# Optimization experiments

Measured on AMD Instinct MI355X. Metric: run time of the kernel, lower is better.

The kernel has to match this reference:

```python
import jax, jax.numpy as jnp
import numpy as np

D_MODEL, N_HEADS, KV_LAT, VOCAB = 2048, 16, 512, 32000
DH = D_MODEL // N_HEADS
ROPE_BASE = 20000.0
LN_EPS = 1e-5


def _layernorm(x, g, b):
    mu = jnp.mean(x, axis=-1, keepdims=True)
    var = jnp.var(x, axis=-1, keepdims=True)
    return (x - mu) * jax.lax.rsqrt(var + LN_EPS) * g + b


def _rope(x):
    # standard half-split rotary embedding over the last dim (d_model), base=20000
    B, S, D = x.shape
    half = D // 2
    inv_freq = 1.0 / (ROPE_BASE ** (jnp.arange(half, dtype=jnp.float32) / half))
    ang = jnp.arange(S, dtype=jnp.float32)[:, None] * inv_freq[None, :]  # [S, half]
    cos, sin = jnp.cos(ang), jnp.sin(ang)
    x1, x2 = x[..., :half], x[..., half:]
    return jnp.concatenate([x1 * cos - x2 * sin, x1 * sin + x2 * cos], axis=-1)


def setup_inputs() -> dict:
    key = jax.random.key(0)
    ks = jax.random.split(key, 10)
    s = 0.02
    return {
        "x": jax.random.normal(ks[0], (1, 2048, D_MODEL), dtype=jnp.float32),
        # Linear weights stored as [in, out] so y = x @ W
        "W_dq": jax.random.normal(ks[1], (D_MODEL, KV_LAT), dtype=jnp.float32) * s,
        "W_dkv": jax.random.normal(ks[2], (D_MODEL, KV_LAT), dtype=jnp.float32) * s,
        "W_uk": jax.random.normal(ks[3], (KV_LAT, D_MODEL), dtype=jnp.float32) * s,
        "W_uv": jax.random.normal(ks[4], (KV_LAT, D_MODEL), dtype=jnp.float32) * s,
        "W_uq": jax.random.normal(ks[5], (KV_LAT, D_MODEL), dtype=jnp.float32) * s,
        "W_qr": jax.random.normal(ks[6], (KV_LAT, D_MODEL), dtype=jnp.float32) * s,
        "W_kr": jax.random.normal(ks[7], (D_MODEL, DH), dtype=jnp.float32) * s,
        "W_o": jax.random.normal(ks[8], (D_MODEL, VOCAB), dtype=jnp.float32) * s,
        "g_kv": jnp.ones((KV_LAT,), dtype=jnp.float32),
        "b_kv": jnp.zeros((KV_LAT,), dtype=jnp.float32),
        "g_kr": jnp.ones((DH,), dtype=jnp.float32),
        "b_kr": jnp.zeros((DH,), dtype=jnp.float32),
    }


def reference(x, W_dq, W_dkv, W_uk, W_uv, W_uq, W_qr, W_kr, W_o,
              g_kv, b_kv, g_kr, b_kr):
    B, S, D = x.shape
    # query latent and up-projection
    c_q = _layernorm(x @ W_dq, g_kv, b_kv)                      # [B,S,kv]
    q_c = (c_q @ W_uq).reshape(B, S, N_HEADS, DH)               # [B,S,H,dh]
    # kv latent cache (no past cache -> just this chunk)
    c_kv = _layernorm(x @ W_dkv, g_kv, b_kv)                    # [B,S,kv]
    k_c = (c_kv @ W_uk).reshape(B, S, N_HEADS, DH)
    v_c = (c_kv @ W_uv).reshape(B, S, N_HEADS, DH)
    # decoupled RoPE paths (RoPE applied only to q, as in source)
    q_r = _rope(c_q @ W_qr).reshape(B, S, N_HEADS, DH)
    k_r = _layernorm(x @ W_kr, g_kr, b_kr)                      # [B,S,dh]
    k_r_h = jnp.broadcast_to(k_r[:, :, None, :], (B, S, N_HEADS, DH))
    q = jnp.concatenate([q_c, q_r], axis=3)                     # [B,S,H,2dh]
    k = jnp.concatenate([k_c, k_r_h], axis=3)                   # [B,S,H,2dh]
    scores = jnp.einsum("bqhd,bkhd->bhqk", q, k) / np.sqrt(2.0 * DH)
    causal = jnp.tril(jnp.ones((S, S), dtype=bool))             # past_length=0
    scores = jnp.where(causal[None, None], scores, -jnp.inf)
    attn = jax.nn.softmax(scores, axis=-1)
    out_heads = jnp.einsum("bhqk,bkhd->bqhd", attn, v_c).reshape(B, S, D)
    out = out_heads @ W_o                                       # [B,S,vocab]
    return out, c_kv, k_r_h
```

## Files before the change

kernel.cpp:

```cpp
#include <hip/hip_runtime.h>


typedef __bf16 bf16;
typedef __bf16 bf16x8 __attribute__((ext_vector_type(8)));
typedef float f32x4 __attribute__((ext_vector_type(4)));

__device__ __forceinline__ unsigned bfbits(float f) {
  unsigned u = __float_as_uint(f);
  return (u + 0x7fffu + ((u >> 16) & 1u)) >> 16;
}
__device__ __forceinline__ bf16 f2bf(float f) {
  union { unsigned short u; bf16 b; } cv;
  cv.u = (unsigned short)bfbits(f);
  return cv.b;
}

__device__ __forceinline__ void async16(const void* g, const void* l) {
  typedef const __attribute__((address_space(1))) unsigned int* gp_t;
  typedef __attribute__((address_space(3))) unsigned int* lp_t;
  __builtin_amdgcn_global_load_lds((gp_t)(unsigned long long)g,
                                   (lp_t)(unsigned int)(unsigned long long)l,
                                   16, 0, 0);
}

__device__ __forceinline__ void storeC(float* p, float v) { *p = v; }
__device__ __forceinline__ void storeC(bf16* p, float v) { *p = f2bf(v); }

__global__ void k_convert(const float* __restrict__ in, bf16* __restrict__ out, int n4) {
  int i = blockIdx.x * 256 + threadIdx.x;
  if (i >= n4) return;
  float4 v = ((const float4*)in)[i];
  unsigned lo = bfbits(v.x) | (bfbits(v.y) << 16);
  unsigned hi = bfbits(v.z) | (bfbits(v.w) << 16);
  ((uint2*)out)[i] = make_uint2(lo, hi);
}

__global__ void k_transpose(const float* __restrict__ in, bf16* __restrict__ out,
                            int R, int C) {
  __shared__ float tile[32][33];
  int bc = blockIdx.x * 32, br = blockIdx.y * 32;
  int tx = threadIdx.x & 31, ty = threadIdx.x >> 5;
#pragma unroll
  for (int i = 0; i < 32; i += 8)
    tile[ty + i][tx] = in[(size_t)(br + ty + i) * C + bc + tx];
  __syncthreads();
#pragma unroll
  for (int i = 0; i < 32; i += 8)
    out[(size_t)(bc + ty + i) * R + br + tx] = f2bf(tile[tx][ty + i]);
}

template <typename OutT, bool TRANS>
__global__ __launch_bounds__(256, 2)
void k_gemm(const bf16* __restrict__ A, const bf16* __restrict__ Bt,
            OutT* __restrict__ C, int M, int N, int K) {
  __shared__ bf16 As[128 * 64];
  __shared__ bf16 Bs[128 * 64];
  const int tid = threadIdx.x;
  const int w = tid >> 6, lane = tid & 63;
  const int lm = lane & 15, quad = lane >> 4;
  const int m0 = blockIdx.x * 128;
  const int n0 = blockIdx.y * 128;
  const int wm = (w >> 1) * 64, wn = (w & 1) * 64;

  f32x4 acc[4][4] = {};
  const int ar = lane >> 3;
  const int ac = (lane & 7) * 8;
  const bf16* Ab = A + (size_t)m0 * K + ac;
  const bf16* Bb = Bt + (size_t)n0 * K + ac;

  for (int k0 = 0; k0 < K; k0 += 64) {
#pragma unroll
    for (int j = 0; j < 4; ++j) {
      int ch = w * 4 + j;
      int row = ch * 8 + ar;
      async16(Ab + (size_t)row * K + k0, &As[ch * 512]);
      async16(Bb + (size_t)row * K + k0, &Bs[ch * 512]);
    }
    __syncthreads();
#pragma unroll
    for (int kk = 0; kk < 2; ++kk) {
      const int colb = kk * 32 + quad * 8;
      bf16x8 af[4], bfr[4];
#pragma unroll
      for (int i = 0; i < 4; ++i)
        af[i] = *(const bf16x8*)&As[(wm + i * 16 + lm) * 64 + colb];
#pragma unroll
      for (int j = 0; j < 4; ++j)
        bfr[j] = *(const bf16x8*)&Bs[(wn + j * 16 + lm) * 64 + colb];
#pragma unroll
      for (int i = 0; i < 4; ++i)
#pragma unroll
        for (int j = 0; j < 4; ++j)
          acc[i][j] = __builtin_amdgcn_mfma_f32_16x16x32_bf16(af[i], bfr[j], acc[i][j], 0, 0, 0);
    }
    __syncthreads();
  }

#pragma unroll
  for (int i = 0; i < 4; ++i) {
#pragma unroll
    for (int j = 0; j < 4; ++j) {
      f32x4 v = acc[i][j];
      const int row = m0 + wm + i * 16 + quad * 4;
      const int col = n0 + wn + j * 16 + lm;
      if constexpr (TRANS) {
        unsigned lo = bfbits(v[0]) | (bfbits(v[1]) << 16);
        unsigned hi = bfbits(v[2]) | (bfbits(v[3]) << 16);
        *(uint2*)((bf16*)C + (size_t)col * M + row) = make_uint2(lo, hi);
      } else {
#pragma unroll
        for (int r = 0; r < 4; ++r)
          storeC(&C[(size_t)(row + r) * N + col], v[r]);
      }
    }
  }
}

__global__ void k_ln(const float* __restrict__ in, const float* __restrict__ g,
                     const float* __restrict__ b, bf16* __restrict__ obf,
                     float* __restrict__ of32, int C, int bcast) {
  const int row = blockIdx.x, tid = threadIdx.x;
  const float* x = in + (size_t)row * C;
  float v[8];
  float s = 0.f, s2 = 0.f;
  int nv = 0;
  for (int c = tid * 4; c < C; c += 256) {
    float4 t = *(const float4*)(x + c);
    v[nv] = t.x; v[nv + 1] = t.y; v[nv + 2] = t.z; v[nv + 3] = t.w;
    s += t.x + t.y + t.z + t.w;
    s2 += t.x * t.x + t.y * t.y + t.z * t.z + t.w * t.w;
    nv += 4;
  }
#pragma unroll
  for (int d = 1; d < 64; d <<= 1) {
    s += __shfl_xor(s, d, 64);
    s2 += __shfl_xor(s2, d, 64);
  }
  const float invC = 1.0f / (float)C;
  const float mu = s * invC;
  const float rstd = rsqrtf(s2 * invC - mu * mu + 1e-5f);
  nv = 0;
  for (int c = tid * 4; c < C; c += 256) {
#pragma unroll
    for (int q = 0; q < 4; ++q) {
      float y = (v[nv + q] - mu) * rstd * g[c + q] + b[c + q];
      obf[(size_t)row * C + c + q] = f2bf(y);
      if (of32) {
        for (int k2 = 0; k2 < bcast; ++k2)
          of32[((size_t)row * bcast + k2) * C + c + q] = y;
      }
    }
    nv += 4;
  }
}

__global__ void k_rope(const float* __restrict__ pre, bf16* __restrict__ out) {
  const int s = blockIdx.x;
  const int j = threadIdx.x * 4;
  const float* rp = pre + (size_t)s * 2048;
  float4 x1 = *(const float4*)(rp + j);
  float4 x2 = *(const float4*)(rp + 1024 + j);
  float a1[4] = {x1.x, x1.y, x1.z, x1.w};
  float a2[4] = {x2.x, x2.y, x2.z, x2.w};
  float o1[4], o2[4];
#pragma unroll
  for (int q = 0; q < 4; ++q) {
    float invf = powf(20000.0f, -((float)(j + q)) * (1.0f / 1024.0f));
    float ang = (float)s * invf;
    float sn, cs;
    sincosf(ang, &sn, &cs);
    o1[q] = a1[q] * cs - a2[q] * sn;
    o2[q] = a1[q] * sn + a2[q] * cs;
  }
  unsigned l1 = bfbits(o1[0]) | (bfbits(o1[1]) << 16);
  unsigned h1 = bfbits(o1[2]) | (bfbits(o1[3]) << 16);
  unsigned l2 = bfbits(o2[0]) | (bfbits(o2[1]) << 16);
  unsigned h2 = bfbits(o2[2]) | (bfbits(o2[3]) << 16);
  *(uint2*)(out + (size_t)s * 2048 + j) = make_uint2(l1, h1);
  *(uint2*)(out + (size_t)s * 2048 + 1024 + j) = make_uint2(l2, h2);
}

__global__ __launch_bounds__(256, 2)
void k_attn(const bf16* __restrict__ q_c, const bf16* __restrict__ q_r,
            const bf16* __restrict__ k_c, const bf16* __restrict__ k_r,
            const bf16* __restrict__ v_t, bf16* __restrict__ out_h) {
  __shared__ bf16 Ks[64 * 256];
  __shared__ bf16 Vs[128 * 64];
  __shared__ bf16 Ps[64 * 64];
  const int tid = threadIdx.x;
  const int w = tid >> 6, lane = tid & 63;
  const int lm = lane & 15, quad = lane >> 4;
  const int qt = 31 - (blockIdx.x >> 4);
  const int h = blockIdx.x & 15;

  const int qrow = qt * 64 + w * 16 + lm;
  bf16x8 qf[8];
#pragma unroll
  for (int c = 0; c < 8; ++c) {
    int d = c * 32 + quad * 8;
    const bf16* src = (d < 128) ? (q_c + (size_t)qrow * 2048 + h * 128 + d)
                                : (q_r + (size_t)qrow * 2048 + h * 128 + d - 128);
    qf[c] = *(const bf16x8*)src;
  }

  f32x4 o[8] = {};
  float mrow[4] = {-3e38f, -3e38f, -3e38f, -3e38f};
  float lrow[4] = {0.f, 0.f, 0.f, 0.f};

  const int ksr = lane >> 5;
  const int ksd = (lane & 31) * 8;
  const int vsr = lane >> 3;
  const int vss = (lane & 7) * 8;

  for (int kt = 0; kt <= qt; ++kt) {
#pragma unroll
    for (int j = 0; j < 8; ++j) {
      int ch = w * 8 + j;
      int srow = ch * 2 + ksr;
      const bf16* src = (ksd < 128)
          ? (k_c + (size_t)(kt * 64 + srow) * 2048 + h * 128 + ksd)
          : (k_r + (size_t)(kt * 64 + srow) * 128 + ksd - 128);
      async16(src, &Ks[ch * 512]);
    }
#pragma unroll
    for (int j = 0; j < 4; ++j) {
      int ch = w * 4 + j;
      int vrow = ch * 8 + vsr;
      async16(v_t + (size_t)(h * 128 + vrow) * 2048 + kt * 64 + vss, &Vs[ch * 512]);
    }
    __syncthreads();

    f32x4 sa[4] = {};
#pragma unroll
    for (int c = 0; c < 8; ++c) {
#pragma unroll
      for (int ks = 0; ks < 4; ++ks) {
        bf16x8 kf = *(const bf16x8*)&Ks[(ks * 16 + lm) * 256 + c * 32 + quad * 8];
        sa[ks] = __builtin_amdgcn_mfma_f32_16x16x32_bf16(qf[c], kf, sa[ks], 0, 0, 0);
      }
    }
#pragma unroll
    for (int ks = 0; ks < 4; ++ks)
#pragma unroll
      for (int r = 0; r < 4; ++r)
        sa[ks][r] *= 0.0625f;
    if (kt == qt) {
#pragma unroll
      for (int ks = 0; ks < 4; ++ks)
#pragma unroll
        for (int r = 0; r < 4; ++r)
          if (ks * 16 + lm > w * 16 + quad * 4 + r) sa[ks][r] = -1e30f;
    }
    float mx[4], alpha[4], rs[4];
#pragma unroll
    for (int r = 0; r < 4; ++r)
      mx[r] = fmaxf(fmaxf(sa[0][r], sa[1][r]), fmaxf(sa[2][r], sa[3][r]));
#pragma unroll
    for (int d = 1; d < 16; d <<= 1)
#pragma unroll
      for (int r = 0; r < 4; ++r)
        mx[r] = fmaxf(mx[r], __shfl_xor(mx[r], d, 64));
#pragma unroll
    for (int r = 0; r < 4; ++r) {
      float mn = fmaxf(mrow[r], mx[r]);
      alpha[r] = __expf(mrow[r] - mn);
      mrow[r] = mn;
      rs[r] = 0.f;
    }
#pragma unroll
    for (int ks = 0; ks < 4; ++ks)
#pragma unroll
      for (int r = 0; r < 4; ++r) {
        float p = __expf(sa[ks][r] - mrow[r]);
        rs[r] += p;
        Ps[(w * 16 + quad * 4 + r) * 64 + ks * 16 + lm] = f2bf(p);
      }
#pragma unroll
    for (int d = 1; d < 16; d <<= 1)
#pragma unroll
      for (int r = 0; r < 4; ++r)
        rs[r] += __shfl_xor(rs[r], d, 64);
#pragma unroll
    for (int r = 0; r < 4; ++r)
      lrow[r] = lrow[r] * alpha[r] + rs[r];
#pragma unroll
    for (int d8 = 0; d8 < 8; ++d8)
#pragma unroll
      for (int r = 0; r < 4; ++r)
        o[d8][r] *= alpha[r];
    __syncthreads();

    bf16x8 pf[2];
#pragma unroll
    for (int kc = 0; kc < 2; ++kc)
      pf[kc] = *(const bf16x8*)&Ps[(w * 16 + lm) * 64 + kc * 32 + quad * 8];
#pragma unroll
    for (int d8 = 0; d8 < 8; ++d8) {
#pragma unroll
      for (int kc = 0; kc < 2; ++kc) {
        bf16x8 vf = *(const bf16x8*)&Vs[(d8 * 16 + lm) * 64 + kc * 32 + quad * 8];
        o[d8] = __builtin_amdgcn_mfma_f32_16x16x32_bf16(pf[kc], vf, o[d8], 0, 0, 0);
      }
    }
    __syncthreads();
  }

  float inv_l[4];
#pragma unroll
  for (int r = 0; r < 4; ++r) inv_l[r] = 1.0f / lrow[r];
  bf16* Os = Ks;
#pragma unroll
  for (int d8 = 0; d8 < 8; ++d8)
#pragma unroll
    for (int r = 0; r < 4; ++r)
      Os[(w * 16 + quad * 4 + r) * 128 + d8 * 16 + lm] = f2bf(o[d8][r] * inv_l[r]);
  __syncthreads();
#pragma unroll
  for (int it = 0; it < 4; ++it) {
    int u = it * 256 + tid;
    int row = u >> 4, cb = u & 15;
    *(uint4*)(out_h + (size_t)(qt * 64 + row) * 2048 + h * 128 + cb * 8) =
        *(const uint4*)&Os[row * 128 + cb * 8];
  }
}

extern "C" void kernel_launch(void* const* d_in, const int* in_sizes, int n_in,
                              void* d_out, int out_size, void* d_ws, size_t ws_size,
                              hipStream_t stream) {
  const float* x    = (const float*)d_in[0];
  const float* Wdq  = (const float*)d_in[1];
  const float* Wdkv = (const float*)d_in[2];
  const float* Wuk  = (const float*)d_in[3];
  const float* Wuv  = (const float*)d_in[4];
  const float* Wuq  = (const float*)d_in[5];
  const float* Wqr  = (const float*)d_in[6];
  const float* Wkr  = (const float*)d_in[7];
  const float* Wo   = (const float*)d_in[8];
  const float* g_kv = (const float*)d_in[9];
  const float* b_kv = (const float*)d_in[10];
  const float* g_kr = (const float*)d_in[11];
  const float* b_kr = (const float*)d_in[12];

  float* out   = (float*)d_out;
  float* o_ckv = out + 65536000;
  float* o_krh = o_ckv + 1048576;

  char* ws = (char*)d_ws;
  const size_t MB = 1ull << 20;
  bf16*  x_bf   = (bf16*)(ws + 0);
  bf16*  WdqT   = (bf16*)(ws + 8 * MB);
  bf16*  WdkvT  = (bf16*)(ws + 10 * MB);
  bf16*  WkrT   = (bf16*)(ws + 12 * MB);
  bf16*  WuqT   = (bf16*)(ws + 13 * MB);
  bf16*  WukT   = (bf16*)(ws + 15 * MB);
  bf16*  WuvT   = (bf16*)(ws + 17 * MB);
  bf16*  WqrT   = (bf16*)(ws + 19 * MB);
  float* a_dq   = (float*)(ws + 21 * MB);
  float* a_dkv  = (float*)(ws + 25 * MB);
  float* a_kr   = (float*)(ws + 29 * MB);
  bf16*  cq_bf  = (bf16*)(ws + 30 * MB);
  bf16*  ckv_bf = (bf16*)(ws + 32 * MB);
  bf16*  kr_bf  = (bf16*)(ws + 34 * MB);
  bf16*  q_c    = (bf16*)(ws + 35 * MB);
  float* qrpre  = (float*)(ws + 43 * MB);
  bf16*  q_r    = (bf16*)(ws + 59 * MB);
  bf16*  k_c    = (bf16*)(ws + 67 * MB);
  bf16*  v_t    = (bf16*)(ws + 75 * MB);
  bf16*  WoT    = (bf16*)(ws + 0);
  bf16*  out_h  = (bf16*)(ws + 126 * MB);

  k_convert<<<4096, 256, 0, stream>>>(x, x_bf, 1048576);
  k_transpose<<<dim3(16, 64), 256, 0, stream>>>(Wdq, WdqT, 2048, 512);
  k_transpose<<<dim3(16, 64), 256, 0, stream>>>(Wdkv, WdkvT, 2048, 512);
  k_transpose<<<dim3(4, 64), 256, 0, stream>>>(Wkr, WkrT, 2048, 128);
  k_transpose<<<dim3(64, 16), 256, 0, stream>>>(Wuq, WuqT, 512, 2048);
  k_transpose<<<dim3(64, 16), 256, 0, stream>>>(Wuk, WukT, 512, 2048);
  k_transpose<<<dim3(64, 16), 256, 0, stream>>>(Wuv, WuvT, 512, 2048);
  k_transpose<<<dim3(64, 16), 256, 0, stream>>>(Wqr, WqrT, 512, 2048);

  k_gemm<float, false><<<dim3(16, 4), 256, 0, stream>>>(x_bf, WdqT, a_dq, 2048, 512, 2048);
  k_gemm<float, false><<<dim3(16, 4), 256, 0, stream>>>(x_bf, WdkvT, a_dkv, 2048, 512, 2048);
  k_gemm<float, false><<<dim3(16, 1), 256, 0, stream>>>(x_bf, WkrT, a_kr, 2048, 128, 2048);

  k_ln<<<2048, 64, 0, stream>>>(a_dq, g_kv, b_kv, cq_bf, (float*)nullptr, 512, 1);
  k_ln<<<2048, 64, 0, stream>>>(a_dkv, g_kv, b_kv, ckv_bf, o_ckv, 512, 1);
  k_ln<<<2048, 64, 0, stream>>>(a_kr, g_kr, b_kr, kr_bf, o_krh, 128, 16);

  k_gemm<bf16, false><<<dim3(16, 16), 256, 0, stream>>>(cq_bf, WuqT, q_c, 2048, 2048, 512);
  k_gemm<float, false><<<dim3(16, 16), 256, 0, stream>>>(cq_bf, WqrT, qrpre, 2048, 2048, 512);
  k_gemm<bf16, false><<<dim3(16, 16), 256, 0, stream>>>(ckv_bf, WukT, k_c, 2048, 2048, 512);
  k_gemm<bf16, true><<<dim3(16, 16), 256, 0, stream>>>(ckv_bf, WuvT, v_t, 2048, 2048, 512);

  k_rope<<<2048, 256, 0, stream>>>(qrpre, q_r);

  k_attn<<<512, 256, 0, stream>>>(q_c, q_r, k_c, kr_bf, v_t, out_h);

  k_transpose<<<dim3(1000, 64), 256, 0, stream>>>(Wo, WoT, 2048, 32000);
  k_gemm<float, false><<<dim3(16, 250), 256, 0, stream>>>(out_h, WoT, out, 2048, 32000, 2048);

  (void)in_sizes; (void)n_in; (void)out_size; (void)ws_size;
}
```

Measured before the change: 1.175 ms.

## Add 256x256 pipelined MFMA GEMM for output projection and fuse down-projections

Introduces a 512-thread GEMM kernel with 256x256 tiles, double-buffered async global-to-LDS loads, XOR-swizzled shared memory and interleaved MFMA phases with priority hints, used for the large vocabulary projection. It also merges the three down-projection GEMMs into one wider GEMM over the contiguous transposed weights, with the layernorm kernels reading strided slices. The aim is to raise data reuse and overlap on the dominant GEMM and to cut launch overhead. It relies on workspace contiguity and on the dimensions dividing the tile sizes.

```diff
diff --git a/kernel.cpp b/kernel.cpp
--- a/kernel.cpp
+++ b/kernel.cpp
@@ -116,11 +116,157 @@
   }
 }
 
+__global__ __launch_bounds__(512, 2)
+void k_gemm256(const bf16* __restrict__ A, const bf16* __restrict__ Bt,
+               float* __restrict__ C, int M, int N, int K) {
+  __shared__ bf16 sh[2][2][256 * 64];
+  const int tid = threadIdx.x;
+  const int lane = tid & 63, lm = lane & 15, quad = lane >> 4;
+  const int wid = tid >> 6, wm = wid >> 2, wn = wid & 3;
+
+  const int mt = M >> 8;
+  const int qq = gridDim.x >> 3;
+  const int swz = (blockIdx.x & 7) * qq + (blockIdx.x >> 3);
+  const int m0 = (swz % mt) * 256, n0 = (swz / mt) * 256;
+  const int NT = K >> 6;
+
+  const int sr = (tid >> 3) & 31;
+  const int sc8 = ((tid & 7) ^ (sr & 7)) << 3;
+  const int shalf = tid >> 8;
+  const int lbase = ((tid >> 6) & 3) * 512;
+  const bf16* Ag = A + (size_t)(m0 + sr) * K + sc8;
+  const bf16* Bg = Bt + (size_t)(n0 + sr) * K + sc8;
+
+  auto stg = [&](const bf16* g, bf16* dst, int R0, int R1, int k0) {
+    const int R = (shalf ? R1 : R0);
+    async16(g + (size_t)R * K + k0, dst + R * 64 + lbase);
+  };
+  auto ldf = [&](const bf16* buf, int row, int col) -> bf16x8 {
+    return *(const bf16x8*)&buf[row * 64 + (col ^ ((row & 7) << 3))];
+  };
+
+  stg(Ag, sh[0][0],   0,  32, 0);  stg(Ag, sh[0][0], 128, 160, 0);
+  stg(Bg, sh[0][1],   0,  64, 0);  stg(Bg, sh[0][1], 128, 192, 0);
+  stg(Bg, sh[0][1],  32,  96, 0);  stg(Bg, sh[0][1], 160, 224, 0);
+  stg(Ag, sh[0][0],  64,  96, 0);  stg(Ag, sh[0][0], 192, 224, 0);
+  if (NT > 1) {
+    stg(Ag, sh[1][0],   0,  32, 64);  stg(Ag, sh[1][0], 128, 160, 64);
+    stg(Bg, sh[1][1],   0,  64, 64);  stg(Bg, sh[1][1], 128, 192, 64);
+    stg(Bg, sh[1][1],  32,  96, 64);  stg(Bg, sh[1][1], 160, 224, 64);
+    asm volatile("s_waitcnt vmcnt(6)" ::: "memory");
+  } else {
+    asm volatile("s_waitcnt vmcnt(0)" ::: "memory");
+  }
+  __builtin_amdgcn_s_barrier();
+
+  f32x4 acc[8][4] = {};
+  for (int u = 0; u < NT; ++u) {
+    const int bu = u & 1;
+    const bf16* pA = sh[bu][0];
+    const bf16* pB = sh[bu][1];
+    bf16* nA = sh[bu ^ 1][0];
+    bf16* cA = sh[bu][0];
+    bf16* cB = sh[bu][1];
+    const int k1 = (u + 1) << 6, k2 = (u + 2) << 6;
+    const bool st1 = (u + 1 < NT), st2 = (u + 2 < NT);
+
+    bf16x8 af[4][2], b0[2][2], b1[2][2];
+
+#pragma unroll
+    for (int mf = 0; mf < 4; ++mf)
+#pragma unroll
+      for (int kk = 0; kk < 2; ++kk)
+        af[mf][kk] = ldf(pA, wm * 128 + mf * 16 + lm, kk * 32 + quad * 8);
+#pragma unroll
+    for (int nf = 0; nf < 2; ++nf)
+#pragma unroll
+      for (int kk = 0; kk < 2; ++kk)
+        b0[nf][kk] = ldf(pB, wn * 64 + nf * 16 + lm, kk * 32 + quad * 8);
+    if (st1) { stg(Ag, nA, 64, 96, k1); stg(Ag, nA, 192, 224, k1); }
+    __builtin_amdgcn_s_barrier();
+    asm volatile("s_waitcnt lgkmcnt(0)" ::: "memory");
+    __builtin_amdgcn_s_setprio(1);
+#pragma unroll
+    for (int mf = 0; mf < 4; ++mf)
+#pragma unroll
+      for (int nf = 0; nf < 2; ++nf)
+#pragma unroll
+        for (int kk = 0; kk < 2; ++kk)
+          acc[mf][nf] = __builtin_amdgcn_mfma_f32_16x16x32_bf16(af[mf][kk], b0[nf][kk], acc[mf][nf], 0, 0, 0);
+    __builtin_amdgcn_s_setprio(0);
+    __builtin_amdgcn_s_barrier();
+
+#pragma unroll
+    for (int nf = 0; nf < 2; ++nf)
+#pragma unroll
+      for (int kk = 0; kk < 2; ++kk)
+        b1[nf][kk] = ldf(pB, wn * 64 + (2 + nf) * 16 + lm, kk * 32 + quad * 8);
+    if (st2) { stg(Ag, cA, 0, 32, k2); stg(Ag, cA, 128, 160, k2); }
+    __builtin_amdgcn_s_barrier();
+    asm volatile("s_waitcnt lgkmcnt(0)" ::: "memory");
+    __builtin_amdgcn_s_setprio(1);
+#pragma unroll
+    for (int mf = 0; mf < 4; ++mf)
+#pragma unroll
+      for (int nf = 0; nf < 2; ++nf)
+#pragma unroll
+        for (int kk = 0; kk < 2; ++kk)
+          acc[mf][2 + nf] = __builtin_amdgcn_mfma_f32_16x16x32_bf16(af[mf][kk], b1[nf][kk], acc[mf][2 + nf], 0, 0, 0);
+    __builtin_amdgcn_s_setprio(0);
+    __builtin_amdgcn_s_barrier();
+
+#pragma unroll
+    for (int mf = 0; mf < 4; ++mf)
+#pragma unroll
+      for (int kk = 0; kk < 2; ++kk)
+        af[mf][kk] = ldf(pA, wm * 128 + (4 + mf) * 16 + lm, kk * 32 + quad * 8);
+    if (st2) { stg(Bg, cB, 0, 64, k2); stg(Bg, cB, 128, 192, k2); }
+    __builtin_amdgcn_s_barrier();
+    asm volatile("s_waitcnt lgkmcnt(0)" ::: "memory");
+    __builtin_amdgcn_s_setprio(1);
+#pragma unroll
+    for (int mf = 0; mf < 4; ++mf)
+#pragma unroll
+      for (int nf = 0; nf < 2; ++nf)
+#pragma unroll
+        for (int kk = 0; kk < 2; ++kk)
+          acc[4 + mf][2 + nf] = __builtin_amdgcn_mfma_f32_16x16x32_bf16(af[mf][kk], b1[nf][kk], acc[4 + mf][2 + nf], 0, 0, 0);
+    __builtin_amdgcn_s_setprio(0);
+    __builtin_amdgcn_s_barrier();
+
+    if (st2) { stg(Bg, cB, 32, 96, k2); stg(Bg, cB, 160, 224, k2); }
+    __builtin_amdgcn_s_barrier();
+    __builtin_amdgcn_s_setprio(1);
+#pragma unroll
+    for (int mf = 0; mf < 4; ++mf)
+#pragma unroll
+      for (int nf = 0; nf < 2; ++nf)
+#pragma unroll
+        for (int kk = 0; kk < 2; ++kk)
+          acc[4 + mf][nf] = __builtin_amdgcn_mfma_f32_16x16x32_bf16(af[mf][kk], b0[nf][kk], acc[4 + mf][nf], 0, 0, 0);
+    __builtin_amdgcn_s_setprio(0);
+    if (u < NT - 2) asm volatile("s_waitcnt vmcnt(6)" ::: "memory");
+    else            asm volatile("s_waitcnt vmcnt(0)" ::: "memory");
+    __builtin_amdgcn_s_barrier();
+  }
+
+#pragma unroll
+  for (int mf = 0; mf < 8; ++mf)
+#pragma unroll
+    for (int nf = 0; nf < 4; ++nf) {
+      const int row = m0 + wm * 128 + mf * 16 + quad * 4;
+      const int col = n0 + wn * 64 + nf * 16 + lm;
+#pragma unroll
+      for (int r = 0; r < 4; ++r)
+        C[(size_t)(row + r) * N + col] = acc[mf][nf][r];
+    }
+}
+
 __global__ void k_ln(const float* __restrict__ in, const float* __restrict__ g,
                      const float* __restrict__ b, bf16* __restrict__ obf,
-                     float* __restrict__ of32, int C, int bcast) {
+                     float* __restrict__ of32, int C, int ldin, int bcast) {
   const int row = blockIdx.x, tid = threadIdx.x;
-  const float* x = in + (size_t)row * C;
+  const float* x = in + (size_t)row * ldin;
   float v[8];
   float s = 0.f, s2 = 0.f;
   int nv = 0;
@@ -355,9 +501,7 @@
   bf16*  WukT   = (bf16*)(ws + 15 * MB);
   bf16*  WuvT   = (bf16*)(ws + 17 * MB);
   bf16*  WqrT   = (bf16*)(ws + 19 * MB);
-  float* a_dq   = (float*)(ws + 21 * MB);
-  float* a_dkv  = (float*)(ws + 25 * MB);
-  float* a_kr   = (float*)(ws + 29 * MB);
+  float* a_all  = (float*)(ws + 21 * MB);
   bf16*  cq_bf  = (bf16*)(ws + 30 * MB);
   bf16*  ckv_bf = (bf16*)(ws + 32 * MB);
   bf16*  kr_bf  = (bf16*)(ws + 34 * MB);
@@ -378,13 +522,11 @@
   k_transpose<<<dim3(64, 16), 256, 0, stream>>>(Wuv, WuvT, 512, 2048);
   k_transpose<<<dim3(64, 16), 256, 0, stream>>>(Wqr, WqrT, 512, 2048);
 
-  k_gemm<float, false><<<dim3(16, 4), 256, 0, stream>>>(x_bf, WdqT, a_dq, 2048, 512, 2048);
-  k_gemm<float, false><<<dim3(16, 4), 256, 0, stream>>>(x_bf, WdkvT, a_dkv, 2048, 512, 2048);
-  k_gemm<float, false><<<dim3(16, 1), 256, 0, stream>>>(x_bf, WkrT, a_kr, 2048, 128, 2048);
-
-  k_ln<<<2048, 64, 0, stream>>>(a_dq, g_kv, b_kv, cq_bf, (float*)nullptr, 512, 1);
-  k_ln<<<2048, 64, 0, stream>>>(a_dkv, g_kv, b_kv, ckv_bf, o_ckv, 512, 1);
-  k_ln<<<2048, 64, 0, stream>>>(a_kr, g_kr, b_kr, kr_bf, o_krh, 128, 16);
+  k_gemm<float, false><<<dim3(16, 9), 256, 0, stream>>>(x_bf, WdqT, a_all, 2048, 1152, 2048);
+
+  k_ln<<<2048, 64, 0, stream>>>(a_all +    0, g_kv, b_kv, cq_bf, (float*)nullptr, 512, 1152, 1);
+  k_ln<<<2048, 64, 0, stream>>>(a_all +  512, g_kv, b_kv, ckv_bf, o_ckv, 512, 1152, 1);
+  k_ln<<<2048, 64, 0, stream>>>(a_all + 1024, g_kr, b_kr, kr_bf, o_krh, 128, 1152, 16);
 
   k_gemm<bf16, false><<<dim3(16, 16), 256, 0, stream>>>(cq_bf, WuqT, q_c, 2048, 2048, 512);
   k_gemm<float, false><<<dim3(16, 16), 256, 0, stream>>>(cq_bf, WqrT, qrpre, 2048, 2048, 512);
@@ -396,7 +538,7 @@
   k_attn<<<512, 256, 0, stream>>>(q_c, q_r, k_c, kr_bf, v_t, out_h);
 
   k_transpose<<<dim3(1000, 64), 256, 0, stream>>>(Wo, WoT, 2048, 32000);
-  k_gemm<float, false><<<dim3(16, 250), 256, 0, stream>>>(out_h, WoT, out, 2048, 32000, 2048);
+  k_gemm256<<<1000, 512, 0, stream>>>(out_h, WoT, out, 2048, 32000, 2048);
 
   (void)in_sizes; (void)n_in; (void)out_size; (void)ws_size;
 }
```

After: 1.022 ms. -13.0%, faster.
